# Optimization experiments

Hardware: AMD Instinct MI355X
Metric: run time of the kernel (lower is better)

## Reference

```python
import jax, jax.numpy as jnp
import numpy as np

N, E = 50000, 800000
IN_C, HID, OUT_C, HEADS = 768, 64, 8, 8
NEG_SLOPE = 0.2
BN_EPS = 1e-5


def _bn(x, g, b, m, v):
    # BatchNorm1d in eval mode with running stats
    return (x - m) * jax.lax.rsqrt(v + BN_EPS) * g + b


def _gat_conv(x, W, att_src, att_dst, bias, src, dst, n):
    H, C = att_src.shape
    xw = (x @ W).reshape(n, H, C)                      # [N,H,C]
    a_src = jnp.sum(xw * att_src, axis=-1)             # [N,H]
    a_dst = jnp.sum(xw * att_dst, axis=-1)             # [N,H]
    alpha = jax.nn.leaky_relu(a_src[src] + a_dst[dst], NEG_SLOPE)  # [E',H]
    amax = jax.ops.segment_max(alpha, dst, num_segments=n)          # [N,H]
    ex = jnp.exp(alpha - amax[dst])
    denom = jax.ops.segment_sum(ex, dst, num_segments=n)            # [N,H]
    coef = ex / denom[dst]                                          # [E',H]
    out = jax.ops.segment_sum(xw[src] * coef[:, :, None], dst, num_segments=n)
    return out.reshape(n, H * C) + bias


def setup_inputs() -> dict:
    key = jax.random.key(0)
    ks = jax.random.split(key, 24)
    d = {}
    d['x'] = jax.random.normal(ks[0], (N, IN_C), dtype=jnp.float32)
    d['edge_index'] = jax.random.randint(ks[1], (2, E), 0, N, dtype=jnp.int32)
    d['proj_W'] = jax.random.normal(ks[2], (IN_C, HID), dtype=jnp.float32) * (IN_C ** -0.5)
    d['proj_b'] = jnp.zeros((HID,), jnp.float32)
    for i, kb in zip((1, 2, 3), (ks[3], ks[4], ks[5])):
        k1, k2 = jax.random.split(kb)
        d[f'bn{i}_g'] = jnp.ones((HID,), jnp.float32)
        d[f'bn{i}_b'] = jnp.zeros((HID,), jnp.float32)
        d[f'bn{i}_m'] = jax.random.normal(k1, (HID,), dtype=jnp.float32) * 0.1
        d[f'bn{i}_v'] = jax.random.uniform(k2, (HID,), dtype=jnp.float32, minval=0.5, maxval=1.5)
    C1 = HID // HEADS
    d['W1'] = jax.random.normal(ks[6], (HID, HEADS * C1), dtype=jnp.float32) * (HID ** -0.5)
    d['att_src1'] = jax.random.normal(ks[7], (HEADS, C1), dtype=jnp.float32) * 0.1
    d['att_dst1'] = jax.random.normal(ks[8], (HEADS, C1), dtype=jnp.float32) * 0.1
    d['b1'] = jnp.zeros((HEADS * C1,), jnp.float32)
    d['W2'] = jax.random.normal(ks[9], (HID, HID), dtype=jnp.float32) * (HID ** -0.5)
    d['att_src2'] = jax.random.normal(ks[10], (1, HID), dtype=jnp.float32) * 0.1
    d['att_dst2'] = jax.random.normal(ks[11], (1, HID), dtype=jnp.float32) * 0.1
    d['b2'] = jnp.zeros((HID,), jnp.float32)
    d['cls_W'] = jax.random.normal(ks[12], (HID, OUT_C), dtype=jnp.float32) * (HID ** -0.5)
    d['cls_b'] = jnp.zeros((OUT_C,), jnp.float32)
    return d


def reference(x, edge_index, proj_W, proj_b,
              bn1_g, bn1_b, bn1_m, bn1_v,
              W1, att_src1, att_dst1, b1,
              bn2_g, bn2_b, bn2_m, bn2_v,
              W2, att_src2, att_dst2, b2,
              bn3_g, bn3_b, bn3_m, bn3_v,
              cls_W, cls_b):
    n = x.shape[0]
    # add self-loops (PyG GATConv default)
    loop = jnp.arange(n, dtype=edge_index.dtype)
    src = jnp.concatenate([edge_index[0], loop])
    dst = jnp.concatenate([edge_index[1], loop])

    h = x @ proj_W + proj_b
    h = jax.nn.elu(_bn(h, bn1_g, bn1_b, bn1_m, bn1_v))
    identity = h
    h = _gat_conv(h, W1, att_src1, att_dst1, b1, src, dst, n)
    h = jax.nn.elu(_bn(h, bn2_g, bn2_b, bn2_m, bn2_v) + identity)
    identity = h
    h = _gat_conv(h, W2, att_src2, att_dst2, b2, src, dst, n)
    h = jax.nn.elu(_bn(h, bn3_g, bn3_b, bn3_m, bn3_v) + identity)
    return h @ cls_W + cls_b
```

## Files before the change

### kernel.cpp

```cpp
#include <hip/hip_runtime.h>

typedef __bf16 bf16;
typedef __attribute__((ext_vector_type(8))) __bf16 bf16x8;
typedef __attribute__((ext_vector_type(4))) float f32x4;

#define LSTR 40
#define BN_EPS 1e-5f

__global__ __launch_bounds__(256) void k_prep(
        const float* __restrict__ W0, const float* __restrict__ W1, const float* __restrict__ W2,
        bf16* __restrict__ Wt0, bf16* __restrict__ Wt1, bf16* __restrict__ Wt2,
        int* __restrict__ cnt, int n)
{
    int i = blockIdx.x*256 + threadIdx.x;
    const int T = 768*64 + 8192;
    if (i < 768*64)            { int k = i>>6, n_ = i&63;                  Wt0[n_*768+k] = (bf16)W0[i]; }
    else if (i < 768*64+4096)  { int j = i-768*64;      int k=j>>6,c=j&63; Wt1[c*64+k]  = (bf16)W1[j]; }
    else if (i < T)            { int j = i-768*64-4096; int k=j>>6,c=j&63; Wt2[c*64+k]  = (bf16)W2[j]; }
    int j = i - T;
    if (j >= 0 && j < n) cnt[j] = 0;
}

template<int MODE, bool ABF, int H>
__global__ __launch_bounds__(256) void k_gemm64(
        const void* __restrict__ Av, const bf16* __restrict__ Bt, int M, int K,
        const float* __restrict__ pb, const float* __restrict__ g, const float* __restrict__ bb,
        const float* __restrict__ mm, const float* __restrict__ vv,
        bf16* __restrict__ outB,
        float* __restrict__ a_s, float* __restrict__ a_d,
        const float* __restrict__ att_s, const float* __restrict__ att_d)
{
    __shared__ bf16 xs[64*LSTR];
    __shared__ bf16 bs[64*LSTR];
    __shared__ float sC[64], cC[64];

    int t = threadIdx.x;
    int w = t >> 6, lane = t & 63;
    int q = lane >> 4, l16 = lane & 15;
    int row0 = blockIdx.x * 64;
    int sRow = t >> 2, sK = (t & 3) * 8;

    auto loadA = [&](int k0) -> bf16x8 {
        bf16x8 xv;
        #pragma unroll
        for (int i = 0; i < 8; ++i) xv[i] = (bf16)0.f;
        int gr = row0 + sRow;
        if (gr < M) {
            if constexpr (ABF) {
                xv = *(const bf16x8*)((const bf16*)Av + (size_t)gr*K + k0 + sK);
            } else {
                const float* ap = (const float*)Av + (size_t)gr*K + k0 + sK;
                float4 f0 = *(const float4*)ap;
                float4 f1 = *(const float4*)(ap + 4);
                xv[0]=(bf16)f0.x; xv[1]=(bf16)f0.y; xv[2]=(bf16)f0.z; xv[3]=(bf16)f0.w;
                xv[4]=(bf16)f1.x; xv[5]=(bf16)f1.y; xv[6]=(bf16)f1.z; xv[7]=(bf16)f1.w;
            }
        }
        return xv;
    };
    auto loadB = [&](int k0) -> bf16x8 {
        return *(const bf16x8*)(Bt + (size_t)sRow*K + k0 + sK);
    };

    f32x4 acc[4];
    #pragma unroll
    for (int i = 0; i < 4; ++i) { acc[i][0]=0.f; acc[i][1]=0.f; acc[i][2]=0.f; acc[i][3]=0.f; }

    bf16x8 xv = loadA(0);
    bf16x8 bv = loadB(0);

    for (int k0 = 0; k0 < K; k0 += 32) {
        *(bf16x8*)(xs + sRow*LSTR + sK) = xv;
        *(bf16x8*)(bs + sRow*LSTR + sK) = bv;
        __syncthreads();
        if (k0 + 32 < K) {
            xv = loadA(k0 + 32);
            bv = loadB(k0 + 32);
        }
        bf16x8 af = *(bf16x8*)(xs + (w*16 + l16)*LSTR + q*8);
        #pragma unroll
        for (int tt = 0; tt < 4; ++tt) {
            bf16x8 bfr = *(bf16x8*)(bs + (tt*16 + l16)*LSTR + q*8);
            acc[tt] = __builtin_amdgcn_mfma_f32_16x16x32_bf16(af, bfr, acc[tt], 0, 0, 0);
        }
        __syncthreads();
    }

    if constexpr (MODE == 0) {
        if (t < 64) {
            float s = rsqrtf(vv[t] + BN_EPS) * g[t];
            sC[t] = s;
            cC[t] = (pb[t] - mm[t]) * s + bb[t];
        }
        __syncthreads();
    }

    #pragma unroll
    for (int tt = 0; tt < 4; ++tt) {
        int col = tt*16 + l16;
        #pragma unroll
        for (int r = 0; r < 4; ++r) {
            int row = row0 + w*16 + q*4 + r;
            if (row < M) {
                float val = acc[tt][r];
                if constexpr (MODE == 0) {
                    val = val * sC[col] + cC[col];
                    val = val > 0.f ? val : __expf(val) - 1.f;
                }
                outB[(size_t)row*64 + col] = (bf16)val;
            }
        }
    }

    if constexpr (MODE == 1) {
        #pragma unroll
        for (int r = 0; r < 4; ++r) {
            int row = row0 + w*16 + q*4 + r;
            if constexpr (H == 1) {
                float ps = 0.f, pd = 0.f;
                #pragma unroll
                for (int tt = 0; tt < 4; ++tt) {
                    int col = tt*16 + l16;
                    ps += acc[tt][r] * att_s[col];
                    pd += acc[tt][r] * att_d[col];
                }
                #pragma unroll
                for (int off = 1; off < 16; off <<= 1) {
                    ps += __shfl_xor(ps, off);
                    pd += __shfl_xor(pd, off);
                }
                if (l16 == 0 && row < M) { a_s[row] = ps; a_d[row] = pd; }
            } else {
                float ps[4], pd[4];
                #pragma unroll
                for (int tt = 0; tt < 4; ++tt) {
                    int col = tt*16 + l16;
                    ps[tt] = acc[tt][r] * att_s[col];
                    pd[tt] = acc[tt][r] * att_d[col];
                }
                #pragma unroll
                for (int off = 1; off < 8; off <<= 1) {
                    #pragma unroll
                    for (int tt = 0; tt < 4; ++tt) {
                        ps[tt] += __shfl_xor(ps[tt], off);
                        pd[tt] += __shfl_xor(pd[tt], off);
                    }
                }
                if ((l16 & 7) == 0 && row < M) {
                    int hb = l16 >> 3;
                    #pragma unroll
                    for (int tt = 0; tt < 4; ++tt) {
                        a_s[row*8 + 2*tt + hb] = ps[tt];
                        a_d[row*8 + 2*tt + hb] = pd[tt];
                    }
                }
            }
        }
    }
}

__global__ __launch_bounds__(256) void k_count(const int* __restrict__ dst, int E, int* cnt) {
    int i = blockIdx.x*256 + threadIdx.x;
    if (i < E) atomicAdd(&cnt[dst[i]], 1);
}
__global__ __launch_bounds__(256) void k_scan_block(const int* __restrict__ cnt,
        int* __restrict__ rp, int* __restrict__ bsum, int n) {
    __shared__ int s[256];
    int t = threadIdx.x, v = blockIdx.x*256 + t;
    int x = (v < n) ? cnt[v] : 0;
    s[t] = x; __syncthreads();
    for (int off = 1; off < 256; off <<= 1) {
        int y = (t >= off) ? s[t-off] : 0;
        __syncthreads();
        s[t] += y;
        __syncthreads();
    }
    if (v < n) rp[v+1] = s[t];
    if (t == 255) bsum[blockIdx.x] = s[255];
}
__global__ __launch_bounds__(256) void k_scan_bsum(int* bsum, int nb) {
    __shared__ int s[256];
    int t = threadIdx.x;
    int x = (t < nb) ? bsum[t] : 0;
    s[t] = x; __syncthreads();
    for (int off = 1; off < 256; off <<= 1) {
        int y = (t >= off) ? s[t-off] : 0;
        __syncthreads();
        s[t] += y;
        __syncthreads();
    }
    if (t < nb) bsum[t] = s[t] - x;
}
__global__ __launch_bounds__(256) void k_finalize(int* __restrict__ rp, const int* __restrict__ bsum,
        const int* __restrict__ cnt, int* __restrict__ cursor, int n) {
    int v = blockIdx.x*256 + threadIdx.x;
    if (v < n) {
        int val = rp[v+1] + bsum[v >> 8];
        rp[v+1] = val;
        cursor[v] = val - cnt[v];
        if (v == 0) rp[0] = 0;
    }
}
__global__ __launch_bounds__(256) void k_scatter(const int* __restrict__ src, const int* __restrict__ dst,
        int E, int* __restrict__ cursor, int* __restrict__ in_src) {
    int i = blockIdx.x*256 + threadIdx.x;
    if (i < E) {
        int pos = atomicAdd(&cursor[dst[i]], 1);
        in_src[pos] = src[i];
    }
}

template<int H, bool CLS>
__global__ __launch_bounds__(256) void k_gat_agg(const bf16* __restrict__ xwb,
        const float* __restrict__ a_src, const float* __restrict__ a_dst,
        const int* __restrict__ rp, const int* __restrict__ in_src,
        const float* __restrict__ bias,
        const float* __restrict__ g, const float* __restrict__ bb,
        const float* __restrict__ mm, const float* __restrict__ vv,
        const bf16* __restrict__ resid, bf16* __restrict__ outB, float* __restrict__ outF,
        const float* __restrict__ clsW, const float* __restrict__ clsb, int n)
{
    int wv = (blockIdx.x*256 + threadIdx.x) >> 6;
    int lane = threadIdx.x & 63;
    if (wv >= n) return;
    int h = (H == 8) ? (lane >> 3) : 0;
    float adst = a_dst[wv*H + h];

    float aself = a_src[wv*H + h] + adst;
    aself = (aself > 0.f) ? aself : 0.2f*aself;
    float eself = __expf(aself);
    float acc = eself * (float)xwb[(size_t)wv*64 + lane];
    float den = eself;

    int beg = rp[wv], end = rp[wv+1];
    int e = beg;
    for (; e + 8 <= end; e += 8) {
        int u[8];
        #pragma unroll
        for (int i = 0; i < 8; ++i) u[i] = in_src[e+i];
        float s[8], xr[8];
        #pragma unroll
        for (int i = 0; i < 8; ++i) s[i] = a_src[u[i]*H + h];
        #pragma unroll
        for (int i = 0; i < 8; ++i) xr[i] = (float)xwb[(size_t)u[i]*64 + lane];
        #pragma unroll
        for (int i = 0; i < 8; ++i) {
            float a = s[i] + adst;
            a = (a > 0.f) ? a : 0.2f*a;
            float ex = __expf(a);
            acc += ex * xr[i];
            den += ex;
        }
    }
    for (; e < end; ++e) {
        int u = in_src[e];
        float al = a_src[u*H + h] + adst;
        al = (al > 0.f) ? al : 0.2f*al;
        float ex = __expf(al);
        acc += ex * (float)xwb[(size_t)u*64 + lane];
        den += ex;
    }
    float val = acc/den + bias[lane];
    float sc = rsqrtf(vv[lane] + BN_EPS) * g[lane];
    val = (val - mm[lane]) * sc + bb[lane];
    val += (float)resid[(size_t)wv*64 + lane];
    val = (val > 0.f) ? val : __expf(val) - 1.f;

    if constexpr (!CLS) {
        outB[(size_t)wv*64 + lane] = (bf16)val;
    } else {
        float keep = 0.f;
        #pragma unroll
        for (int o = 0; o < 8; ++o) {
            float p = val * clsW[lane*8 + o];
            #pragma unroll
            for (int off = 1; off < 64; off <<= 1) p += __shfl_xor(p, off);
            if (lane == o) keep = p + clsb[o];
        }
        if (lane < 8) outF[(size_t)wv*8 + lane] = keep;
    }
}

extern "C" void kernel_launch(void* const* d_in, const int* in_sizes, int n_in,
                              void* d_out, int out_size, void* d_ws, size_t ws_size,
                              hipStream_t stream)
{
    const float* x      = (const float*)d_in[0];
    const int*   ei     = (const int*)  d_in[1];
    const float* proj_W = (const float*)d_in[2];
    const float* proj_b = (const float*)d_in[3];
    const float* bn1_g  = (const float*)d_in[4];
    const float* bn1_b  = (const float*)d_in[5];
    const float* bn1_m  = (const float*)d_in[6];
    const float* bn1_v  = (const float*)d_in[7];
    const float* bn2_g  = (const float*)d_in[8];
    const float* bn2_b  = (const float*)d_in[9];
    const float* bn2_m  = (const float*)d_in[10];
    const float* bn2_v  = (const float*)d_in[11];
    const float* bn3_g  = (const float*)d_in[12];
    const float* bn3_b  = (const float*)d_in[13];
    const float* bn3_m  = (const float*)d_in[14];
    const float* bn3_v  = (const float*)d_in[15];
    const float* W1     = (const float*)d_in[16];
    const float* att_s1 = (const float*)d_in[17];
    const float* att_d1 = (const float*)d_in[18];
    const float* b1     = (const float*)d_in[19];
    const float* W2     = (const float*)d_in[20];
    const float* att_s2 = (const float*)d_in[21];
    const float* att_d2 = (const float*)d_in[22];
    const float* b2     = (const float*)d_in[23];
    const float* cls_W  = (const float*)d_in[24];
    const float* cls_b  = (const float*)d_in[25];

    const int N = in_sizes[0] / 768;
    const int E = in_sizes[1] / 2;
    const int* srce = ei;
    const int* dste = ei + E;

    char* p = (char*)d_ws;
    auto carve = [&](size_t bytes) -> void* {
        void* r = (void*)p;
        p += (bytes + 255) & ~(size_t)255;
        return r;
    };
    bf16*  Wt0    = (bf16*) carve((size_t)64*768*2);
    bf16*  Wt1    = (bf16*) carve((size_t)64*64*2);
    bf16*  Wt2    = (bf16*) carve((size_t)64*64*2);
    bf16*  h0b    = (bf16*) carve((size_t)N*64*2);
    bf16*  h1b    = (bf16*) carve((size_t)N*64*2);
    bf16*  xwb    = (bf16*) carve((size_t)N*64*2);
    float* a_s    = (float*)carve((size_t)N*8*4);
    float* a_d    = (float*)carve((size_t)N*8*4);
    int*   cnt    = (int*)  carve((size_t)N*4);
    int*   rp     = (int*)  carve((size_t)(N+1)*4);
    int*   cursor = (int*)  carve((size_t)N*4);
    int*   bsum   = (int*)  carve(1024);
    int*   in_src = (int*)  carve((size_t)E*4);

    const int nb = (N + 255) / 256;
    const int PREP = 768*64 + 8192;

    k_prep<<<(PREP + N + 255)/256, 256, 0, stream>>>(proj_W, W1, W2, Wt0, Wt1, Wt2, cnt, N);

    k_count<<<(E + 255)/256, 256, 0, stream>>>(dste, E, cnt);
    k_scan_block<<<nb, 256, 0, stream>>>(cnt, rp, bsum, N);
    k_scan_bsum<<<1, 256, 0, stream>>>(bsum, nb);
    k_finalize<<<nb, 256, 0, stream>>>(rp, bsum, cnt, cursor, N);
    k_scatter<<<(E + 255)/256, 256, 0, stream>>>(srce, dste, E, cursor, in_src);

    k_gemm64<0, false, 1><<<(N + 63)/64, 256, 0, stream>>>(x, Wt0, N, 768,
            proj_b, bn1_g, bn1_b, bn1_m, bn1_v, h0b, nullptr, nullptr, nullptr, nullptr);

    k_gemm64<1, true, 8><<<(N + 63)/64, 256, 0, stream>>>(h0b, Wt1, N, 64,
            nullptr, nullptr, nullptr, nullptr, nullptr, xwb, a_s, a_d, att_s1, att_d1);
    k_gat_agg<8, false><<<(N + 3)/4, 256, 0, stream>>>(xwb, a_s, a_d, rp, in_src,
            b1, bn2_g, bn2_b, bn2_m, bn2_v, h0b, h1b, nullptr, nullptr, nullptr, N);

    k_gemm64<1, true, 1><<<(N + 63)/64, 256, 0, stream>>>(h1b, Wt2, N, 64,
            nullptr, nullptr, nullptr, nullptr, nullptr, xwb, a_s, a_d, att_s2, att_d2);
    k_gat_agg<1, true><<<(N + 3)/4, 256, 0, stream>>>(xwb, a_s, a_d, rp, in_src,
            b2, bn3_g, bn3_b, bn3_m, bn3_v, h1b, nullptr, (float*)d_out, cls_W, cls_b, N);
}
```

Before: 499.7 us.

## Split GAT aggregation wavefront into four edge-parallel sub-groups with vectorized bf16x4 loads

Rewrites the per-node aggregation so each wavefront splits into four 16-lane groups. Each lane handles four channels through bf16x4 loads, and the four groups walk disjoint neighbor edges, with the self-loop folded in as virtual edge 0. Partial sums are combined with cross-lane shuffles, and the classifier reduction shrinks to 16 lanes. This exposes more independent gathers per wavefront for the memory-latency-bound neighbor loop, at the cost of redundant attention-score loads and exp computations per edge within each 16-lane group, plus a shuffle reduction at the end.

```diff
diff --git a/kernel.cpp b/kernel.cpp
--- a/kernel.cpp
+++ b/kernel.cpp
@@ -1,6 +1,7 @@
 #include <hip/hip_runtime.h>
 
 typedef __bf16 bf16;
+typedef __attribute__((ext_vector_type(4))) __bf16 bf16x4;
 typedef __attribute__((ext_vector_type(8))) __bf16 bf16x8;
 typedef __attribute__((ext_vector_type(4))) float f32x4;
 
@@ -223,61 +224,82 @@
     int wv = (blockIdx.x*256 + threadIdx.x) >> 6;
     int lane = threadIdx.x & 63;
     if (wv >= n) return;
-    int h = (H == 8) ? (lane >> 3) : 0;
+    int sub = lane >> 4, j = lane & 15;
+    int h = (H == 8) ? (j >> 1) : 0;
     float adst = a_dst[wv*H + h];
 
-    float aself = a_src[wv*H + h] + adst;
-    aself = (aself > 0.f) ? aself : 0.2f*aself;
-    float eself = __expf(aself);
-    float acc = eself * (float)xwb[(size_t)wv*64 + lane];
-    float den = eself;
-
-    int beg = rp[wv], end = rp[wv+1];
-    int e = beg;
-    for (; e + 8 <= end; e += 8) {
-        int u[8];
-        #pragma unroll
-        for (int i = 0; i < 8; ++i) u[i] = in_src[e+i];
-        float s[8], xr[8];
-        #pragma unroll
-        for (int i = 0; i < 8; ++i) s[i] = a_src[u[i]*H + h];
-        #pragma unroll
-        for (int i = 0; i < 8; ++i) xr[i] = (float)xwb[(size_t)u[i]*64 + lane];
-        #pragma unroll
-        for (int i = 0; i < 8; ++i) {
-            float a = s[i] + adst;
-            a = (a > 0.f) ? a : 0.2f*a;
-            float ex = __expf(a);
-            acc += ex * xr[i];
-            den += ex;
-        }
-    }
-    for (; e < end; ++e) {
-        int u = in_src[e];
-        float al = a_src[u*H + h] + adst;
-        al = (al > 0.f) ? al : 0.2f*al;
-        float ex = __expf(al);
-        acc += ex * (float)xwb[(size_t)u*64 + lane];
-        den += ex;
-    }
-    float val = acc/den + bias[lane];
-    float sc = rsqrtf(vv[lane] + BN_EPS) * g[lane];
-    val = (val - mm[lane]) * sc + bb[lane];
-    val += (float)resid[(size_t)wv*64 + lane];
-    val = (val > 0.f) ? val : __expf(val) - 1.f;
+    int beg = rp[wv];
+    int cntv = rp[wv+1] - beg + 1;
+
+    float acc0=0.f, acc1=0.f, acc2=0.f, acc3=0.f, den=0.f;
+    int vi = sub;
+    for (; vi + 4 < cntv; vi += 8) {
+        int u0 = (vi == 0) ? wv : in_src[beg + vi - 1];
+        int u1 = in_src[beg + vi + 3];
+        float s0 = a_src[u0*H + h];
+        float s1 = a_src[u1*H + h];
+        bf16x4 q0 = *(const bf16x4*)(xwb + (size_t)u0*64 + 4*j);
+        bf16x4 q1 = *(const bf16x4*)(xwb + (size_t)u1*64 + 4*j);
+        float a0 = s0 + adst; a0 = (a0 > 0.f) ? a0 : 0.2f*a0; float e0 = __expf(a0);
+        float a1 = s1 + adst; a1 = (a1 > 0.f) ? a1 : 0.2f*a1; float e1 = __expf(a1);
+        acc0 += e0*(float)q0[0] + e1*(float)q1[0];
+        acc1 += e0*(float)q0[1] + e1*(float)q1[1];
+        acc2 += e0*(float)q0[2] + e1*(float)q1[2];
+        acc3 += e0*(float)q0[3] + e1*(float)q1[3];
+        den  += e0 + e1;
+    }
+    if (vi < cntv) {
+        int u0 = (vi == 0) ? wv : in_src[beg + vi - 1];
+        float s0 = a_src[u0*H + h];
+        bf16x4 q0 = *(const bf16x4*)(xwb + (size_t)u0*64 + 4*j);
+        float a0 = s0 + adst; a0 = (a0 > 0.f) ? a0 : 0.2f*a0; float e0 = __expf(a0);
+        acc0 += e0*(float)q0[0];
+        acc1 += e0*(float)q0[1];
+        acc2 += e0*(float)q0[2];
+        acc3 += e0*(float)q0[3];
+        den  += e0;
+    }
+    #pragma unroll
+    for (int off = 16; off < 64; off <<= 1) {
+        acc0 += __shfl_xor(acc0, off);
+        acc1 += __shfl_xor(acc1, off);
+        acc2 += __shfl_xor(acc2, off);
+        acc3 += __shfl_xor(acc3, off);
+        den  += __shfl_xor(den,  off);
+    }
+
+    int c0 = 4*j;
+    bf16x4 rq = *(const bf16x4*)(resid + (size_t)wv*64 + c0);
+    float val[4] = {acc0, acc1, acc2, acc3};
+    #pragma unroll
+    for (int i = 0; i < 4; ++i) {
+        int c = c0 + i;
+        float sc = rsqrtf(vv[c] + BN_EPS) * g[c];
+        float v = val[i]/den + bias[c];
+        v = (v - mm[c]) * sc + bb[c];
+        v += (float)rq[i];
+        val[i] = (v > 0.f) ? v : __expf(v) - 1.f;
+    }
 
     if constexpr (!CLS) {
-        outB[(size_t)wv*64 + lane] = (bf16)val;
+        if (sub == 0) {
+            bf16x4 ov;
+            #pragma unroll
+            for (int i = 0; i < 4; ++i) ov[i] = (bf16)val[i];
+            *(bf16x4*)(outB + (size_t)wv*64 + c0) = ov;
+        }
     } else {
         float keep = 0.f;
         #pragma unroll
         for (int o = 0; o < 8; ++o) {
-            float p = val * clsW[lane*8 + o];
+            float p = 0.f;
             #pragma unroll
-            for (int off = 1; off < 64; off <<= 1) p += __shfl_xor(p, off);
-            if (lane == o) keep = p + clsb[o];
-        }
-        if (lane < 8) outF[(size_t)wv*8 + lane] = keep;
+            for (int i = 0; i < 4; ++i) p += val[i] * clsW[(c0+i)*8 + o];
+            #pragma unroll
+            for (int off = 1; off < 16; off <<= 1) p += __shfl_xor(p, off);
+            if (j == o) keep = p + clsb[o];
+        }
+        if (sub == 0 && j < 8) outF[(size_t)wv*8 + j] = keep;
     }
 }
 
```

Measured after the change: 629.6 us. 1.26x slower.

## Split GAT feature tables into column halves and aggregate in two passes

Applied to the files above, without the earlier changes.

The GEMM epilogue now writes the transformed features and attention logits as separate low and high 32-column halves. Each GAT aggregation runs as two launches, one per half. Each wave processes two edges at once, one per half-wave, and the halves are combined with a cross-lane shuffle. The smaller per-pass gather tables are meant to fit better in cache and to make better use of each gathered row. In exchange the edge-index and logit reads are repeated per pass, launches are added, and the classifier output is accumulated with a read-modify-write in the second pass.

```diff
diff --git a/kernel.cpp b/kernel.cpp
--- a/kernel.cpp
+++ b/kernel.cpp
@@ -27,7 +27,9 @@
         const float* __restrict__ pb, const float* __restrict__ g, const float* __restrict__ bb,
         const float* __restrict__ mm, const float* __restrict__ vv,
         bf16* __restrict__ outB,
-        float* __restrict__ a_s, float* __restrict__ a_d,
+        bf16* __restrict__ xwLo, bf16* __restrict__ xwHi,
+        float* __restrict__ asLo, float* __restrict__ asHi,
+        float* __restrict__ adLo, float* __restrict__ adHi,
         const float* __restrict__ att_s, const float* __restrict__ att_d)
 {
     __shared__ bf16 xs[64*LSTR];
@@ -106,8 +108,11 @@
                 if constexpr (MODE == 0) {
                     val = val * sC[col] + cC[col];
                     val = val > 0.f ? val : __expf(val) - 1.f;
-                }
-                outB[(size_t)row*64 + col] = (bf16)val;
+                    outB[(size_t)row*64 + col] = (bf16)val;
+                } else {
+                    if (col < 32) xwLo[(size_t)row*32 + col]      = (bf16)val;
+                    else          xwHi[(size_t)row*32 + col - 32] = (bf16)val;
+                }
             }
         }
     }
@@ -129,7 +134,7 @@
                     ps += __shfl_xor(ps, off);
                     pd += __shfl_xor(pd, off);
                 }
-                if (l16 == 0 && row < M) { a_s[row] = ps; a_d[row] = pd; }
+                if (l16 == 0 && row < M) { asLo[row] = ps; adLo[row] = pd; }
             } else {
                 float ps[4], pd[4];
                 #pragma unroll
@@ -150,8 +155,9 @@
                     int hb = l16 >> 3;
                     #pragma unroll
                     for (int tt = 0; tt < 4; ++tt) {
-                        a_s[row*8 + 2*tt + hb] = ps[tt];
-                        a_d[row*8 + 2*tt + hb] = pd[tt];
+                        int head = 2*tt + hb;
+                        if (head < 4) { asLo[row*4 + head]     = ps[tt]; adLo[row*4 + head]     = pd[tt]; }
+                        else          { asHi[row*4 + head - 4] = ps[tt]; adHi[row*4 + head - 4] = pd[tt]; }
                     }
                 }
             }
@@ -210,8 +216,8 @@
     }
 }
 
-template<int H, bool CLS>
-__global__ __launch_bounds__(256) void k_gat_agg(const bf16* __restrict__ xwb,
+template<int H, bool CLS, int PASS>
+__global__ __launch_bounds__(256) void k_gat_agg(const bf16* __restrict__ xwh,
         const float* __restrict__ a_src, const float* __restrict__ a_dst,
         const int* __restrict__ rp, const int* __restrict__ in_src,
         const float* __restrict__ bias,
@@ -223,61 +229,74 @@
     int wv = (blockIdx.x*256 + threadIdx.x) >> 6;
     int lane = threadIdx.x & 63;
     if (wv >= n) return;
-    int h = (H == 8) ? (lane >> 3) : 0;
-    float adst = a_dst[wv*H + h];
-
-    float aself = a_src[wv*H + h] + adst;
-    aself = (aself > 0.f) ? aself : 0.2f*aself;
-    float eself = __expf(aself);
-    float acc = eself * (float)xwb[(size_t)wv*64 + lane];
-    float den = eself;
+    int half = lane >> 5, f = lane & 31;
+    int hh = (H == 8) ? (f >> 3) : 0;
+    float adst = (H == 8) ? a_dst[wv*4 + hh] : a_dst[wv];
+
+    float acc = 0.f, den = 0.f;
+    if (half == 0) {
+        float as = (H == 8) ? a_src[wv*4 + hh] : a_src[wv];
+        float a = as + adst; a = (a > 0.f) ? a : 0.2f*a;
+        float ex = __expf(a);
+        acc = ex * (float)xwh[(size_t)wv*32 + f];
+        den = ex;
+    }
 
     int beg = rp[wv], end = rp[wv+1];
-    int e = beg;
-    for (; e + 8 <= end; e += 8) {
-        int u[8];
-        #pragma unroll
-        for (int i = 0; i < 8; ++i) u[i] = in_src[e+i];
-        float s[8], xr[8];
-        #pragma unroll
-        for (int i = 0; i < 8; ++i) s[i] = a_src[u[i]*H + h];
-        #pragma unroll
-        for (int i = 0; i < 8; ++i) xr[i] = (float)xwb[(size_t)u[i]*64 + lane];
-        #pragma unroll
-        for (int i = 0; i < 8; ++i) {
-            float a = s[i] + adst;
-            a = (a > 0.f) ? a : 0.2f*a;
-            float ex = __expf(a);
-            acc += ex * xr[i];
-            den += ex;
-        }
-    }
-    for (; e < end; ++e) {
-        int u = in_src[e];
-        float al = a_src[u*H + h] + adst;
-        al = (al > 0.f) ? al : 0.2f*al;
-        float ex = __expf(al);
-        acc += ex * (float)xwb[(size_t)u*64 + lane];
+    int idx = beg + half;
+    for (; idx + 6 < end; idx += 8) {
+        int u0 = in_src[idx], u1 = in_src[idx+2], u2 = in_src[idx+4], u3 = in_src[idx+6];
+        float s0, s1, s2, s3;
+        if (H == 8) {
+            s0 = a_src[u0*4 + hh]; s1 = a_src[u1*4 + hh];
+            s2 = a_src[u2*4 + hh]; s3 = a_src[u3*4 + hh];
+        } else {
+            s0 = a_src[u0]; s1 = a_src[u1]; s2 = a_src[u2]; s3 = a_src[u3];
+        }
+        float x0 = (float)xwh[(size_t)u0*32 + f];
+        float x1 = (float)xwh[(size_t)u1*32 + f];
+        float x2 = (float)xwh[(size_t)u2*32 + f];
+        float x3 = (float)xwh[(size_t)u3*32 + f];
+        float a0 = s0 + adst; a0 = (a0 > 0.f) ? a0 : 0.2f*a0; float e0 = __expf(a0);
+        float a1 = s1 + adst; a1 = (a1 > 0.f) ? a1 : 0.2f*a1; float e1 = __expf(a1);
+        float a2 = s2 + adst; a2 = (a2 > 0.f) ? a2 : 0.2f*a2; float e2 = __expf(a2);
+        float a3 = s3 + adst; a3 = (a3 > 0.f) ? a3 : 0.2f*a3; float e3 = __expf(a3);
+        acc += e0*x0 + e1*x1 + e2*x2 + e3*x3;
+        den += e0 + e1 + e2 + e3;
+    }
+    for (; idx < end; idx += 2) {
+        int u = in_src[idx];
+        float s = (H == 8) ? a_src[u*4 + hh] : a_src[u];
+        float a = s + adst; a = (a > 0.f) ? a : 0.2f*a;
+        float ex = __expf(a);
+        acc += ex * (float)xwh[(size_t)u*32 + f];
         den += ex;
     }
-    float val = acc/den + bias[lane];
-    float sc = rsqrtf(vv[lane] + BN_EPS) * g[lane];
-    val = (val - mm[lane]) * sc + bb[lane];
-    val += (float)resid[(size_t)wv*64 + lane];
+    acc += __shfl_xor(acc, 32);
+    den += __shfl_xor(den, 32);
+
+    int c = PASS*32 + f;
+    float val = acc/den + bias[c];
+    float sc = rsqrtf(vv[c] + BN_EPS) * g[c];
+    val = (val - mm[c]) * sc + bb[c];
+    val += (float)resid[(size_t)wv*64 + c];
     val = (val > 0.f) ? val : __expf(val) - 1.f;
 
     if constexpr (!CLS) {
-        outB[(size_t)wv*64 + lane] = (bf16)val;
+        if (half == 0) outB[(size_t)wv*64 + c] = (bf16)val;
     } else {
         float keep = 0.f;
         #pragma unroll
         for (int o = 0; o < 8; ++o) {
-            float p = val * clsW[lane*8 + o];
+            float p = val * clsW[c*8 + o];
             #pragma unroll
-            for (int off = 1; off < 64; off <<= 1) p += __shfl_xor(p, off);
-            if (lane == o) keep = p + clsb[o];
-        }
-        if (lane < 8) outF[(size_t)wv*8 + lane] = keep;
+            for (int off = 1; off < 32; off <<= 1) p += __shfl_xor(p, off);
+            if (f == o) keep = p;
+        }
+        if (half == 0 && f < 8) {
+            if (PASS == 0) outF[(size_t)wv*8 + f] = keep + clsb[f];
+            else           outF[(size_t)wv*8 + f] += keep;
+        }
     }
 }
 
@@ -328,9 +347,12 @@
     bf16*  Wt2    = (bf16*) carve((size_t)64*64*2);
     bf16*  h0b    = (bf16*) carve((size_t)N*64*2);
     bf16*  h1b    = (bf16*) carve((size_t)N*64*2);
-    bf16*  xwb    = (bf16*) carve((size_t)N*64*2);
-    float* a_s    = (float*)carve((size_t)N*8*4);
-    float* a_d    = (float*)carve((size_t)N*8*4);
+    bf16*  xwLo   = (bf16*) carve((size_t)N*32*2);
+    bf16*  xwHi   = (bf16*) carve((size_t)N*32*2);
+    float* as0    = (float*)carve((size_t)N*4*4);
+    float* as1    = (float*)carve((size_t)N*4*4);
+    float* ad0    = (float*)carve((size_t)N*4*4);
+    float* ad1    = (float*)carve((size_t)N*4*4);
     int*   cnt    = (int*)  carve((size_t)N*4);
     int*   rp     = (int*)  carve((size_t)(N+1)*4);
     int*   cursor = (int*)  carve((size_t)N*4);
@@ -338,6 +360,7 @@
     int*   in_src = (int*)  carve((size_t)E*4);
 
     const int nb = (N + 255) / 256;
+    const int nw = (N + 3) / 4;
     const int PREP = 768*64 + 8192;
 
     k_prep<<<(PREP + N + 255)/256, 256, 0, stream>>>(proj_W, W1, W2, Wt0, Wt1, Wt2, cnt, N);
@@ -349,15 +372,22 @@
     k_scatter<<<(E + 255)/256, 256, 0, stream>>>(srce, dste, E, cursor, in_src);
 
     k_gemm64<0, false, 1><<<(N + 63)/64, 256, 0, stream>>>(x, Wt0, N, 768,
-            proj_b, bn1_g, bn1_b, bn1_m, bn1_v, h0b, nullptr, nullptr, nullptr, nullptr);
+            proj_b, bn1_g, bn1_b, bn1_m, bn1_v, h0b,
+            nullptr, nullptr, nullptr, nullptr, nullptr, nullptr, nullptr, nullptr);
 
     k_gemm64<1, true, 8><<<(N + 63)/64, 256, 0, stream>>>(h0b, Wt1, N, 64,
-            nullptr, nullptr, nullptr, nullptr, nullptr, xwb, a_s, a_d, att_s1, att_d1);
-    k_gat_agg<8, false><<<(N + 3)/4, 256, 0, stream>>>(xwb, a_s, a_d, rp, in_src,
+            nullptr, nullptr, nullptr, nullptr, nullptr, nullptr,
+            xwLo, xwHi, as0, as1, ad0, ad1, att_s1, att_d1);
+    k_gat_agg<8, false, 0><<<nw, 256, 0, stream>>>(xwLo, as0, ad0, rp, in_src,
             b1, bn2_g, bn2_b, bn2_m, bn2_v, h0b, h1b, nullptr, nullptr, nullptr, N);
+    k_gat_agg<8, false, 1><<<nw, 256, 0, stream>>>(xwHi, as1, ad1, rp, in_src,
+            b1, bn2_g, bn2_b, bn2_m, bn2_v, h0b, h1b, nullptr, nullptr, nullptr, N);
 
     k_gemm64<1, true, 1><<<(N + 63)/64, 256, 0, stream>>>(h1b, Wt2, N, 64,
-            nullptr, nullptr, nullptr, nullptr, nullptr, xwb, a_s, a_d, att_s2, att_d2);
-    k_gat_agg<1, true><<<(N + 3)/4, 256, 0, stream>>>(xwb, a_s, a_d, rp, in_src,
+            nullptr, nullptr, nullptr, nullptr, nullptr, nullptr,
+            xwLo, xwHi, as0, nullptr, ad0, nullptr, att_s2, att_d2);
+    k_gat_agg<1, true, 0><<<nw, 256, 0, stream>>>(xwLo, as0, ad0, rp, in_src,
             b2, bn3_g, bn3_b, bn3_m, bn3_v, h1b, nullptr, (float*)d_out, cls_W, cls_b, N);
-}
+    k_gat_agg<1, true, 1><<<nw, 256, 0, stream>>>(xwHi, as0, ad0, rp, in_src,
+            b2, bn3_g, bn3_b, bn3_m, bn3_v, h1b, nullptr, (float*)d_out, cls_W, cls_b, N);
+}
```

Result: slower. 519.8 us (+4.0%).
